# Kernel tuning notes

Measured on AMD Instinct MI355X. Metric: run time of the kernel, lower is better.

The kernel has to match this reference:

```python
import jax, jax.numpy as jnp
import numpy as np

# Screen constants (from init_kwargs)
RES_X, RES_Y = 1024, 1024          # camera resolution (width, height)
PIX_X, PIX_Y = 1e-5, 1e-5          # pixel size in meters
BINNING = 1
NX, NY = RES_X // BINNING, RES_Y // BINNING  # effective resolution
LEFT, RIGHT = -RES_X * PIX_X / 2.0, RES_X * PIX_X / 2.0
BOTTOM, TOP = -RES_Y * PIX_Y / 2.0, RES_Y * PIX_Y / 2.0
HSTEP, VSTEP = PIX_X * BINNING, PIX_Y * BINNING
N_PARTICLES = 16_777_216
BEAM_SIGMA = 1e-3  # 1 mm rms beam size, fits in +/-5.12 mm screen extent


def setup_inputs() -> dict:
    key = jax.random.key(0)
    kx, ky = jax.random.split(key)
    xs = jax.random.normal(kx, (N_PARTICLES,), dtype=jnp.float32) * BEAM_SIGMA
    ys = jax.random.normal(ky, (N_PARTICLES,), dtype=jnp.float32) * BEAM_SIGMA
    misalignment = jnp.zeros((2,), dtype=jnp.float32)
    return {"xs": xs, "ys": ys, "misalignment": misalignment}


def reference(xs, ys, misalignment):
    # track(): subtract screen misalignment from transverse positions
    x = xs - misalignment[0]
    y = ys - misalignment[1]
    # reading(): 2D histogram over uniform pixel bin edges (torch.histogramdd)
    ix = jnp.floor((x - LEFT) / HSTEP).astype(jnp.int32)
    iy = jnp.floor((y - BOTTOM) / VSTEP).astype(jnp.int32)
    # points exactly on the rightmost/topmost edge belong to the last bin
    ix = jnp.where(x == RIGHT, NX - 1, ix)
    iy = jnp.where(y == TOP, NY - 1, iy)
    valid = (x >= LEFT) & (x <= RIGHT) & (y >= BOTTOM) & (y <= TOP)
    ix = jnp.clip(ix, 0, NX - 1)
    iy = jnp.clip(iy, 0, NY - 1)
    # image = flipud(hist.T): hist is (nx, ny) -> image[NY-1-iy, ix]
    flat = (NY - 1 - iy) * NX + ix
    w = valid.astype(jnp.float32)
    image = jnp.zeros((NY * NX,), dtype=jnp.float32).at[flat].add(w)
    return image.reshape(NY, NX)
```

## Files before the change

kernel.cpp:

```cpp
#include <hip/hip_runtime.h>
#include <hip/hip_bf16.h>


#define NXX 1024
#define NYY 1024
#define NROWS 1024
#define K3_THREADS 512
#define K3_CHUNK 8192
#define K3_G4 (K3_CHUNK / 4)
#define HCOPIES 8
#define HSTRIDE 1025

static __device__ __forceinline__ unsigned int row_of(float y) {
    const float BOTTOM = (float)(-1024.0 * 1e-5 / 2.0);
    const float TOP    = (float)( 1024.0 * 1e-5 / 2.0);
    const float VSTEP  = 1e-5f;
    int iy = (int)floorf((y - BOTTOM) / VSTEP);
    if (y == TOP) iy = NYY - 1;
    bool yvalid = (y >= BOTTOM) & (y <= TOP);
    iy = min(max(iy, 0), NYY - 1);
    if (!yvalid) return 0xFFFFFFFFu;
    return (unsigned int)((NYY - 1) - iy);
}

static __device__ __forceinline__ unsigned int key_of32(float x, float y) {
    unsigned int r = row_of(y);
    if (r == 0xFFFFFFFFu) return 0xFFFFFFFFu;
    const float LEFT  = (float)(-1024.0 * 1e-5 / 2.0);
    const float RIGHT = (float)( 1024.0 * 1e-5 / 2.0);
    const float HSTEP = 1e-5f;
    int ix = (int)floorf((x - LEFT) / HSTEP);
    if (x == RIGHT) ix = NXX - 1;
    bool xvalid = (x >= LEFT) & (x <= RIGHT);
    ix = min(max(ix, 0), NXX - 1);
    unsigned int col = xvalid ? (unsigned int)ix : 0xFFFFu;
    return (r << 16) | col;
}

__global__ __launch_bounds__(512) void k0_init(
    unsigned long long* __restrict__ cursors64, unsigned int cap) {
    int t = threadIdx.x;
    unsigned long long lo = (unsigned long long)((unsigned)(2 * t) * cap);
    unsigned long long hi = (unsigned long long)((unsigned)(2 * t + 1) * cap);
    cursors64[t] = lo | (hi << 32);
}

__global__ __launch_bounds__(256) void k1_count(
    const float4* __restrict__ ys4, const float* __restrict__ mis,
    unsigned long long* __restrict__ counts64, int n4) {
    __shared__ unsigned int lc[2 * NROWS];
    const int t = threadIdx.x;
    #pragma unroll
    for (int j = 0; j < 8; ++j) lc[t + j * 256] = 0u;
    __syncthreads();
    const unsigned int cp = (t & 1) << 10;
    const float my = mis[1];
    for (int i = blockIdx.x * blockDim.x + t; i < n4; i += gridDim.x * blockDim.x) {
        float4 yv = ys4[i];
        unsigned int r;
        r = row_of(yv.x - my); if (r != 0xFFFFFFFFu) atomicAdd(&lc[cp + r], 1u);
        r = row_of(yv.y - my); if (r != 0xFFFFFFFFu) atomicAdd(&lc[cp + r], 1u);
        r = row_of(yv.z - my); if (r != 0xFFFFFFFFu) atomicAdd(&lc[cp + r], 1u);
        r = row_of(yv.w - my); if (r != 0xFFFFFFFFu) atomicAdd(&lc[cp + r], 1u);
    }
    __syncthreads();
    #pragma unroll
    for (int p = 0; p < 2; ++p) {
        unsigned int e = lc[4 * t + 2 * p] + lc[1024 + 4 * t + 2 * p];
        unsigned int o = lc[4 * t + 2 * p + 1] + lc[1024 + 4 * t + 2 * p + 1];
        if (e | o) atomicAdd(&counts64[2 * t + p],
                             (unsigned long long)e | ((unsigned long long)o << 32));
    }
}

__global__ __launch_bounds__(1024) void k2_prefix(
    const unsigned int* __restrict__ counts,
    unsigned int* __restrict__ offsets, unsigned long long* __restrict__ cursors64) {
    __shared__ unsigned int waveSums[16], waveBase[16];
    __shared__ unsigned int sB[NROWS];
    const int t = threadIdx.x, lane = t & 63, wid = t >> 6;
    unsigned int c = counts[t];
    unsigned int incl = c;
    #pragma unroll
    for (int d = 1; d < 64; d <<= 1) {
        unsigned int v = __shfl_up(incl, d, 64);
        if (lane >= d) incl += v;
    }
    if (lane == 63) waveSums[wid] = incl;
    __syncthreads();
    if (t == 0) {
        unsigned int s = 0;
        #pragma unroll
        for (int i = 0; i < 16; ++i) { waveBase[i] = s; s += waveSums[i]; }
    }
    __syncthreads();
    unsigned int excl = waveBase[wid] + incl - c;
    offsets[t] = excl;
    sB[t] = excl;
    __syncthreads();
    if (t < NROWS / 2) {
        cursors64[t] = (unsigned long long)sB[2 * t] |
                       ((unsigned long long)sB[2 * t + 1] << 32);
    }
}

__global__ __launch_bounds__(K3_THREADS) void k3_scatter(
    const float4* __restrict__ xs4, const float4* __restrict__ ys4,
    const float* __restrict__ mis, unsigned long long* __restrict__ cursors64,
    unsigned short* __restrict__ keys, unsigned int cap) {
    __shared__ unsigned int lCount[NROWS];
    __shared__ unsigned int lOff[NROWS];
    __shared__ unsigned int lAdj[NROWS];
    __shared__ unsigned int waveSums[8], waveBase[8];
    __shared__ unsigned int totalKeys;
    __shared__ unsigned int reorder[K3_CHUNK];

    const int t = threadIdx.x, lane = t & 63, wid = t >> 6;
    lCount[t] = 0u; lCount[t + 512] = 0u;
    __syncthreads();
    const float mx = mis[0], my = mis[1];

    const int base4 = blockIdx.x * K3_G4;
    unsigned int mykey[16];
    unsigned short myrank[16];

    #pragma unroll
    for (int j = 0; j < 4; ++j) {
        int i = base4 + j * K3_THREADS + t;
        float4 xv = xs4[i], yv = ys4[i];
        #pragma unroll
        for (int e = 0; e < 4; ++e) {
            float xx = (e == 0 ? xv.x : e == 1 ? xv.y : e == 2 ? xv.z : xv.w) - mx;
            float yy = (e == 0 ? yv.x : e == 1 ? yv.y : e == 2 ? yv.z : yv.w) - my;
            unsigned int k = key_of32(xx, yy);
            mykey[j * 4 + e] = k;
            unsigned int rk = 0;
            if (k != 0xFFFFFFFFu) rk = atomicAdd(&lCount[k >> 16], 1u);
            myrank[j * 4 + e] = (unsigned short)rk;
        }
    }
    __syncthreads();

    unsigned int c0 = lCount[2 * t], c1 = lCount[2 * t + 1];
    unsigned int tsum = c0 + c1;
    unsigned int incl = tsum;
    #pragma unroll
    for (int d = 1; d < 64; d <<= 1) {
        unsigned int v = __shfl_up(incl, d, 64);
        if (lane >= d) incl += v;
    }
    if (lane == 63) waveSums[wid] = incl;
    __syncthreads();
    if (t == 0) {
        unsigned int s = 0;
        #pragma unroll
        for (int i = 0; i < 8; ++i) { waveBase[i] = s; s += waveSums[i]; }
        totalKeys = s;
    }
    __syncthreads();
    unsigned int excl = waveBase[wid] + incl - tsum;
    lOff[2 * t] = excl;
    lOff[2 * t + 1] = excl + c0;
    if (tsum) {
        unsigned long long old = atomicAdd(&cursors64[t],
            (unsigned long long)c0 | ((unsigned long long)c1 << 32));
        lAdj[2 * t]     = (unsigned int)old - excl;
        lAdj[2 * t + 1] = (unsigned int)(old >> 32) - (excl + c0);
    }
    __syncthreads();

    #pragma unroll
    for (int j = 0; j < 16; ++j) {
        unsigned int k = mykey[j];
        if (k != 0xFFFFFFFFu) {
            unsigned int row = k >> 16;
            reorder[lOff[row] + myrank[j]] = k;
        }
    }
    __syncthreads();

    const unsigned int total = totalKeys;
    if (cap == 0) {
        for (unsigned int j = t; j < total; j += K3_THREADS) {
            unsigned int k = reorder[j];
            keys[lAdj[k >> 16] + j] = (unsigned short)k;
        }
    } else {
        for (unsigned int j = t; j < total; j += K3_THREADS) {
            unsigned int k = reorder[j];
            unsigned int row = k >> 16;
            unsigned int g = lAdj[row] + j;
            if (g < (row + 1) * cap) keys[g] = (unsigned short)k;
        }
    }
}

__global__ __launch_bounds__(512) void k4_hist(
    const unsigned short* __restrict__ keys,
    const unsigned int* __restrict__ cnts_or_curs,
    const unsigned int* __restrict__ offsets,
    float* __restrict__ out, unsigned int cap) {
    __shared__ unsigned int hist[HCOPIES * HSTRIDE];
    const int b = blockIdx.x;
    const int r = (b & 1) ? (512 + (b >> 1)) : (511 - (b >> 1));
    for (int t = threadIdx.x; t < HCOPIES * HSTRIDE; t += 512) hist[t] = 0u;
    __syncthreads();
    unsigned int start, cnt;
    if (cap == 0) { start = offsets[r]; cnt = cnts_or_curs[r]; }
    else { start = (unsigned int)r * cap; cnt = cnts_or_curs[r] - start;
           if (cnt > cap) cnt = cap; }
    const unsigned int copy = (threadIdx.x & (HCOPIES - 1)) * HSTRIDE;
    const unsigned int lead = (start & 1u) & (cnt > 0 ? 1u : 0u);
    if (threadIdx.x == 0 && lead) {
        unsigned int c = keys[start];
        if (c < (unsigned int)NXX) atomicAdd(&hist[copy + c], 1u);
    }
    const unsigned int m = cnt - lead;
    const unsigned int* pk = (const unsigned int*)(keys + start + lead);
    const unsigned int pairs = m >> 1;
    for (unsigned int p = threadIdx.x; p < pairs; p += 512) {
        unsigned int v = pk[p];
        unsigned int ca = v & 0xFFFFu, cb = v >> 16;
        if (ca < (unsigned int)NXX) atomicAdd(&hist[copy + ca], 1u);
        if (cb < (unsigned int)NXX) atomicAdd(&hist[copy + cb], 1u);
    }
    if (threadIdx.x == 0 && (m & 1u)) {
        unsigned int c = keys[start + lead + m - 1];
        if (c < (unsigned int)NXX) atomicAdd(&hist[copy + c], 1u);
    }
    __syncthreads();
    float* dst = out + (size_t)r * NXX;
    for (int v = threadIdx.x; v < NXX; v += 512) {
        unsigned int s = 0u;
        #pragma unroll
        for (int c2 = 0; c2 < HCOPIES; ++c2) s += hist[c2 * HSTRIDE + v];
        dst[v] = (float)s;
    }
}

__global__ __launch_bounds__(256) void fallback_hist(
    const float4* __restrict__ xs4, const float4* __restrict__ ys4,
    const float* __restrict__ mis, unsigned int* __restrict__ out, int n4) {
    const float mx = mis[0], my = mis[1];
    int i = blockIdx.x * blockDim.x + threadIdx.x;
    if (i >= n4) return;
    float4 xv = xs4[i], yv = ys4[i];
    #pragma unroll
    for (int e = 0; e < 4; ++e) {
        float xx = (e == 0 ? xv.x : e == 1 ? xv.y : e == 2 ? xv.z : xv.w) - mx;
        float yy = (e == 0 ? yv.x : e == 1 ? yv.y : e == 2 ? yv.z : yv.w) - my;
        unsigned int k = key_of32(xx, yy);
        if (k != 0xFFFFFFFFu && (k & 0xFFFFu) < NXX)
            atomicAdd(&out[(k >> 16) * NXX + (k & 0xFFFFu)], 1u);
    }
}
__global__ __launch_bounds__(256) void convert_kernel(unsigned int* __restrict__ buf, int n) {
    int i = blockIdx.x * blockDim.x + threadIdx.x;
    if (i < n) { unsigned int c = buf[i]; ((float*)buf)[i] = (float)c; }
}

extern "C" void kernel_launch(void* const* d_in, const int* in_sizes, int n_in,
                              void* d_out, int out_size, void* d_ws, size_t ws_size,
                              hipStream_t stream) {
    const float* xs  = (const float*)d_in[0];
    const float* ys  = (const float*)d_in[1];
    const float* mis = (const float*)d_in[2];

    const int n  = in_sizes[0];
    const int n4 = n / 4;

    unsigned char* ws = (unsigned char*)d_ws;
    unsigned int* counts          = (unsigned int*)(ws);
    unsigned long long* counts64  = (unsigned long long*)(ws);
    unsigned int* offsets         = (unsigned int*)(ws + 4096);
    unsigned long long* cursors64 = (unsigned long long*)(ws + 8192);
    unsigned int* cursors32       = (unsigned int*)(ws + 8192);
    unsigned short* keys          = (unsigned short*)(ws + 65536);

    unsigned int cap = 0;
    if (ws_size > 65536) {
        size_t c = (ws_size - 65536) / (NROWS * sizeof(unsigned short));
        c &= ~(size_t)63;
        if (c >= 73728) cap = (unsigned int)((c > 131072) ? 131072 : c);
    }

    const int k3_grid = n / K3_CHUNK;

    if (cap) {
        k0_init<<<1, 512, 0, stream>>>(cursors64, cap);
        k3_scatter<<<k3_grid, K3_THREADS, 0, stream>>>(
            (const float4*)xs, (const float4*)ys, mis, cursors64, keys, cap);
        k4_hist<<<NROWS, 512, 0, stream>>>(keys, cursors32, offsets,
                                           (float*)d_out, cap);
        return;
    }

    const size_t exact_need = 65536 + (size_t)n * sizeof(unsigned short);
    if (ws_size < exact_need) {
        unsigned int* out_u = (unsigned int*)d_out;
        hipMemsetAsync(d_out, 0, (size_t)out_size * sizeof(float), stream);
        fallback_hist<<<(n4 + 255) / 256, 256, 0, stream>>>(
            (const float4*)xs, (const float4*)ys, mis, out_u, n4);
        const int npix = NXX * NYY;
        convert_kernel<<<(npix + 255) / 256, 256, 0, stream>>>(out_u, npix);
        return;
    }

    hipMemsetAsync(ws, 0, 4096, stream);
    k1_count<<<512, 256, 0, stream>>>((const float4*)ys, mis, counts64, n4);
    k2_prefix<<<1, 1024, 0, stream>>>(counts, offsets, cursors64);
    k3_scatter<<<k3_grid, K3_THREADS, 0, stream>>>(
        (const float4*)xs, (const float4*)ys, mis, cursors64, keys, 0u);
    k4_hist<<<NROWS, 512, 0, stream>>>(keys, counts, offsets, (float*)d_out, 0u);
}
```

Measured before the change: 206.0 us.

## Split LDS row counters by parity, pad row segments, widen key stores and histogram loads

Key computation now multiplies by a reciprocal with round-down conversion instead of dividing and flooring, and it checks validity first. The scatter kernel keeps two LDS counters per row, chosen by thread parity, to reduce atomic contention. In the capped path it pads each row's segment to an even length with invalid keys so keys can be written as 32-bit pairs. The histogram kernel moves to 1024 threads and reads keys four at a time as uint2 with head and tail handling. The reciprocal multiply may round differently from the exact divide at bin edges, and the padding adds dummy keys that the histogram must skip.

```diff
diff --git a/kernel.cpp b/kernel.cpp
--- a/kernel.cpp
+++ b/kernel.cpp
@@ -14,12 +14,10 @@
 static __device__ __forceinline__ unsigned int row_of(float y) {
     const float BOTTOM = (float)(-1024.0 * 1e-5 / 2.0);
     const float TOP    = (float)( 1024.0 * 1e-5 / 2.0);
-    const float VSTEP  = 1e-5f;
-    int iy = (int)floorf((y - BOTTOM) / VSTEP);
-    if (y == TOP) iy = NYY - 1;
-    bool yvalid = (y >= BOTTOM) & (y <= TOP);
+    const float INVV   = 1.0f / 1e-5f;
+    if (!((y >= BOTTOM) & (y <= TOP))) return 0xFFFFFFFFu;
+    int iy = __float2int_rd((y - BOTTOM) * INVV);
     iy = min(max(iy, 0), NYY - 1);
-    if (!yvalid) return 0xFFFFFFFFu;
     return (unsigned int)((NYY - 1) - iy);
 }
 
@@ -28,12 +26,14 @@
     if (r == 0xFFFFFFFFu) return 0xFFFFFFFFu;
     const float LEFT  = (float)(-1024.0 * 1e-5 / 2.0);
     const float RIGHT = (float)( 1024.0 * 1e-5 / 2.0);
-    const float HSTEP = 1e-5f;
-    int ix = (int)floorf((x - LEFT) / HSTEP);
-    if (x == RIGHT) ix = NXX - 1;
-    bool xvalid = (x >= LEFT) & (x <= RIGHT);
-    ix = min(max(ix, 0), NXX - 1);
-    unsigned int col = xvalid ? (unsigned int)ix : 0xFFFFu;
+    const float INVH  = 1.0f / 1e-5f;
+    unsigned int col;
+    if ((x >= LEFT) & (x <= RIGHT)) {
+        int ix = __float2int_rd((x - LEFT) * INVH);
+        col = (unsigned int)min(max(ix, 0), NXX - 1);
+    } else {
+        col = 0xFFFFu;
+    }
     return (r << 16) | col;
 }
 
@@ -108,17 +108,18 @@
     const float4* __restrict__ xs4, const float4* __restrict__ ys4,
     const float* __restrict__ mis, unsigned long long* __restrict__ cursors64,
     unsigned short* __restrict__ keys, unsigned int cap) {
-    __shared__ unsigned int lCount[NROWS];
-    __shared__ unsigned int lOff[NROWS];
+    __shared__ unsigned int lCount2[2 * NROWS];
     __shared__ unsigned int lAdj[NROWS];
     __shared__ unsigned int waveSums[8], waveBase[8];
     __shared__ unsigned int totalKeys;
     __shared__ unsigned int reorder[K3_CHUNK];
 
     const int t = threadIdx.x, lane = t & 63, wid = t >> 6;
-    lCount[t] = 0u; lCount[t + 512] = 0u;
+    lCount2[t] = 0u; lCount2[t + 512] = 0u;
+    lCount2[t + 1024] = 0u; lCount2[t + 1536] = 0u;
     __syncthreads();
     const float mx = mis[0], my = mis[1];
+    const unsigned int par = (unsigned int)(t & 1);
 
     const int base4 = blockIdx.x * K3_G4;
     unsigned int mykey[16];
@@ -135,14 +136,19 @@
             unsigned int k = key_of32(xx, yy);
             mykey[j * 4 + e] = k;
             unsigned int rk = 0;
-            if (k != 0xFFFFFFFFu) rk = atomicAdd(&lCount[k >> 16], 1u);
+            if (k != 0xFFFFFFFFu)
+                rk = atomicAdd(&lCount2[((k >> 16) << 1) | par], 1u);
             myrank[j * 4 + e] = (unsigned short)rk;
         }
     }
     __syncthreads();
 
-    unsigned int c0 = lCount[2 * t], c1 = lCount[2 * t + 1];
-    unsigned int tsum = c0 + c1;
+    uint4 c4 = *(const uint4*)&lCount2[4 * t];
+    unsigned int cr0 = c4.x + c4.y, cr1 = c4.z + c4.w;
+    unsigned int p0 = (cap != 0u) ? (cr0 & 1u) : 0u;
+    unsigned int p1 = (cap != 0u) ? (cr1 & 1u) : 0u;
+    unsigned int t0 = cr0 + p0, t1 = cr1 + p1;
+    unsigned int tsum = t0 + t1;
     unsigned int incl = tsum;
     #pragma unroll
     for (int d = 1; d < 64; d <<= 1) {
@@ -158,23 +164,29 @@
         totalKeys = s;
     }
     __syncthreads();
-    unsigned int excl = waveBase[wid] + incl - tsum;
-    lOff[2 * t] = excl;
-    lOff[2 * t + 1] = excl + c0;
+    unsigned int base = waveBase[wid] + incl - tsum;
+    uint4 e4;
+    e4.x = base;
+    e4.y = base + c4.x;
+    e4.z = base + t0;
+    e4.w = base + t0 + c4.z;
+    *(uint4*)&lCount2[4 * t] = e4;
     if (tsum) {
         unsigned long long old = atomicAdd(&cursors64[t],
-            (unsigned long long)c0 | ((unsigned long long)c1 << 32));
-        lAdj[2 * t]     = (unsigned int)old - excl;
-        lAdj[2 * t + 1] = (unsigned int)(old >> 32) - (excl + c0);
-    }
+            (unsigned long long)t0 | ((unsigned long long)t1 << 32));
+        lAdj[2 * t]     = (unsigned int)old - e4.x;
+        lAdj[2 * t + 1] = (unsigned int)(old >> 32) - e4.z;
+    }
+    if (p0) reorder[e4.x + cr0] = ((unsigned int)(2 * t) << 16) | 0xFFFFu;
+    if (p1) reorder[e4.z + cr1] = ((unsigned int)(2 * t + 1) << 16) | 0xFFFFu;
     __syncthreads();
 
     #pragma unroll
     for (int j = 0; j < 16; ++j) {
         unsigned int k = mykey[j];
         if (k != 0xFFFFFFFFu) {
-            unsigned int row = k >> 16;
-            reorder[lOff[row] + myrank[j]] = k;
+            unsigned int idx = ((k >> 16) << 1) | par;
+            reorder[lCount2[idx] + myrank[j]] = k;
         }
     }
     __syncthreads();
@@ -186,16 +198,19 @@
             keys[lAdj[k >> 16] + j] = (unsigned short)k;
         }
     } else {
-        for (unsigned int j = t; j < total; j += K3_THREADS) {
-            unsigned int k = reorder[j];
-            unsigned int row = k >> 16;
-            unsigned int g = lAdj[row] + j;
-            if (g < (row + 1) * cap) keys[g] = (unsigned short)k;
+        const unsigned int pairs = total >> 1;
+        for (unsigned int p = t; p < pairs; p += K3_THREADS) {
+            uint2 kk = *(const uint2*)&reorder[2 * p];
+            unsigned int row = kk.x >> 16;
+            unsigned int g = lAdj[row] + 2 * p;
+            unsigned int val = (kk.x & 0xFFFFu) | (kk.y << 16);
+            if (g + 2 <= (row + 1) * cap)
+                *(unsigned int*)&keys[g] = val;
         }
     }
 }
 
-__global__ __launch_bounds__(512) void k4_hist(
+__global__ __launch_bounds__(1024) void k4_hist(
     const unsigned short* __restrict__ keys,
     const unsigned int* __restrict__ cnts_or_curs,
     const unsigned int* __restrict__ offsets,
@@ -203,34 +218,39 @@
     __shared__ unsigned int hist[HCOPIES * HSTRIDE];
     const int b = blockIdx.x;
     const int r = (b & 1) ? (512 + (b >> 1)) : (511 - (b >> 1));
-    for (int t = threadIdx.x; t < HCOPIES * HSTRIDE; t += 512) hist[t] = 0u;
+    for (int t = threadIdx.x; t < HCOPIES * HSTRIDE; t += 1024) hist[t] = 0u;
     __syncthreads();
     unsigned int start, cnt;
     if (cap == 0) { start = offsets[r]; cnt = cnts_or_curs[r]; }
     else { start = (unsigned int)r * cap; cnt = cnts_or_curs[r] - start;
            if (cnt > cap) cnt = cap; }
     const unsigned int copy = (threadIdx.x & (HCOPIES - 1)) * HSTRIDE;
-    const unsigned int lead = (start & 1u) & (cnt > 0 ? 1u : 0u);
-    if (threadIdx.x == 0 && lead) {
-        unsigned int c = keys[start];
+    unsigned int head = (4u - (start & 3u)) & 3u;
+    if (head > cnt) head = cnt;
+    if (threadIdx.x < head) {
+        unsigned int c = keys[start + threadIdx.x];
         if (c < (unsigned int)NXX) atomicAdd(&hist[copy + c], 1u);
     }
-    const unsigned int m = cnt - lead;
-    const unsigned int* pk = (const unsigned int*)(keys + start + lead);
-    const unsigned int pairs = m >> 1;
-    for (unsigned int p = threadIdx.x; p < pairs; p += 512) {
-        unsigned int v = pk[p];
-        unsigned int ca = v & 0xFFFFu, cb = v >> 16;
-        if (ca < (unsigned int)NXX) atomicAdd(&hist[copy + ca], 1u);
-        if (cb < (unsigned int)NXX) atomicAdd(&hist[copy + cb], 1u);
-    }
-    if (threadIdx.x == 0 && (m & 1u)) {
-        unsigned int c = keys[start + lead + m - 1];
+    const unsigned int m = cnt - head;
+    const uint2* pk = (const uint2*)(keys + start + head);
+    const unsigned int quads = m >> 2;
+    for (unsigned int q = threadIdx.x; q < quads; q += 1024) {
+        uint2 v = pk[q];
+        unsigned int c0 = v.x & 0xFFFFu, c1 = v.x >> 16;
+        unsigned int c2 = v.y & 0xFFFFu, c3 = v.y >> 16;
+        if (c0 < (unsigned int)NXX) atomicAdd(&hist[copy + c0], 1u);
+        if (c1 < (unsigned int)NXX) atomicAdd(&hist[copy + c1], 1u);
+        if (c2 < (unsigned int)NXX) atomicAdd(&hist[copy + c2], 1u);
+        if (c3 < (unsigned int)NXX) atomicAdd(&hist[copy + c3], 1u);
+    }
+    const unsigned int tail = m & 3u;
+    if (threadIdx.x < tail) {
+        unsigned int c = keys[start + head + (quads << 2) + threadIdx.x];
         if (c < (unsigned int)NXX) atomicAdd(&hist[copy + c], 1u);
     }
     __syncthreads();
     float* dst = out + (size_t)r * NXX;
-    for (int v = threadIdx.x; v < NXX; v += 512) {
+    for (int v = threadIdx.x; v < NXX; v += 1024) {
         unsigned int s = 0u;
         #pragma unroll
         for (int c2 = 0; c2 < HCOPIES; ++c2) s += hist[c2 * HSTRIDE + v];
@@ -290,8 +310,8 @@
         k0_init<<<1, 512, 0, stream>>>(cursors64, cap);
         k3_scatter<<<k3_grid, K3_THREADS, 0, stream>>>(
             (const float4*)xs, (const float4*)ys, mis, cursors64, keys, cap);
-        k4_hist<<<NROWS, 512, 0, stream>>>(keys, cursors32, offsets,
-                                           (float*)d_out, cap);
+        k4_hist<<<NROWS, 1024, 0, stream>>>(keys, cursors32, offsets,
+                                            (float*)d_out, cap);
         return;
     }
 
@@ -311,5 +331,5 @@
     k2_prefix<<<1, 1024, 0, stream>>>(counts, offsets, cursors64);
     k3_scatter<<<k3_grid, K3_THREADS, 0, stream>>>(
         (const float4*)xs, (const float4*)ys, mis, cursors64, keys, 0u);
-    k4_hist<<<NROWS, 512, 0, stream>>>(keys, counts, offsets, (float*)d_out, 0u);
-}
+    k4_hist<<<NROWS, 1024, 0, stream>>>(keys, counts, offsets, (float*)d_out, 0u);
+}
```

Result: faster. 197.4 us (-4.2%).
